# Kernel optimization log

Measured on AMD Instinct MI355X. Metric: run time of the kernel, lower is better.

The kernel has to match this reference:

```python
import jax, jax.numpy as jnp
import numpy as np


def _maxpool2x2(t):
    # t: [B, C, H, W] -> [B, C, H//2, W//2]
    b, c, h, w = t.shape
    return t.reshape(b, c, h // 2, 2, w // 2, 2).max(axis=(3, 5))


def setup_inputs() -> dict:
    key = jax.random.key(0)
    ks = jax.random.split(key, 6)
    B, C, H, W = 16, 64, 64, 64
    x = jax.random.normal(ks[0], (B, C, H, W), dtype=jnp.float32)
    # 1x1 conv weights (no bias), stored as [out_ch, in_ch]
    s = 0.05
    W_theta = jax.random.normal(ks[1], (C // 8, C), dtype=jnp.float32) * s
    W_phi = jax.random.normal(ks[2], (C // 8, C), dtype=jnp.float32) * s
    W_g = jax.random.normal(ks[3], (C // 2, C), dtype=jnp.float32) * s
    W_attn = jax.random.normal(ks[4], (C, C // 2), dtype=jnp.float32) * s
    sigma = jnp.ones((1,), dtype=jnp.float32) * 0.5  # nonzero so attn path matters
    return {"x": x, "W_theta": W_theta, "W_phi": W_phi, "W_g": W_g,
            "W_attn": W_attn, "sigma": sigma}


def reference(x, W_theta, W_phi, W_g, W_attn, sigma):
    B, C, H, W = x.shape
    N = H * W
    M = N // 4
    # 1x1 convs are channel matmuls
    theta = jnp.einsum('oc,bchw->bohw', W_theta, x).reshape(B, C // 8, N)      # [B, C/8, N]
    phi = _maxpool2x2(jnp.einsum('oc,bchw->bohw', W_phi, x)).reshape(B, C // 8, M)  # [B, C/8, M]
    attn = jax.nn.softmax(jnp.einsum('bkn,bkm->bnm', theta, phi), axis=-1)    # [B, N, M]
    g = _maxpool2x2(jnp.einsum('oc,bchw->bohw', W_g, x)).reshape(B, C // 2, M)  # [B, C/2, M]
    attn_g = jnp.einsum('bgm,bnm->bgn', g, attn).reshape(B, C // 2, H, W)      # [B, C/2, H, W]
    attn_g = jnp.einsum('oc,bchw->bohw', W_attn, attn_g)                        # [B, C, H, W]
    return x + sigma * attn_g
```

## Files before the change

kernel.cpp:

```cpp
#include <hip/hip_runtime.h>
#include <hip/hip_bf16.h>

#define CC 64
#define NN 4096
#define MM 1024

typedef __attribute__((ext_vector_type(4))) short s4b;
typedef __attribute__((ext_vector_type(8))) short s8b;
typedef __attribute__((ext_vector_type(4))) float float4v;

__device__ inline unsigned short f2bf(float f) {
    union { float f; unsigned u; } v; v.f = f;
    unsigned r = v.u + 0x7fff + ((v.u >> 16) & 1);
    return (unsigned short)(r >> 16);
}

__device__ inline float4v mfma16(s4b a, s4b b, float4v c) {
#if __has_builtin(__builtin_amdgcn_mfma_f32_16x16x16bf16_1k)
    return __builtin_amdgcn_mfma_f32_16x16x16bf16_1k(a, b, c, 0, 0, 0);
#else
    float4v d;
    asm volatile("v_mfma_f32_16x16x16_bf16 %0, %1, %2, %3"
                 : "=v"(d) : "v"(a), "v"(b), "v"(c));
    return d;
#endif
}

__device__ inline float4v mfma32(s8b a, s8b b, float4v c) {
#if __has_builtin(__builtin_amdgcn_mfma_f32_16x16x32_bf16)
    return __builtin_amdgcn_mfma_f32_16x16x32_bf16(a, b, c, 0, 0, 0);
#else
    float4v d;
    asm volatile("v_mfma_f32_16x16x32_bf16 %0, %1, %2, %3"
                 : "=v"(d) : "v"(a), "v"(b), "v"(c));
    return d;
#endif
}

__global__ __launch_bounds__(256) void prep_kernel(
    const float* __restrict__ x,
    const float* __restrict__ Wth,
    const float* __restrict__ Wph,
    const float* __restrict__ Wg,
    unsigned short* __restrict__ thT,
    unsigned short* __restrict__ phiP,
    unsigned short* __restrict__ gP)
{
    __shared__ float wt[64 * 48];
    __shared__ float buf[128 * 49];

    const int tid  = threadIdx.x;
    const int b    = blockIdx.y;
    const int hp   = blockIdx.x;
    const int pix  = tid & 127;
    const int half = tid >> 7;

    for (int idx = tid; idx < 64 * 48; idx += 256) {
        const int c = idx / 48, j = idx % 48;
        float v;
        if (j < 8)       v = Wth[j * 64 + c];
        else if (j < 16) v = Wph[(j - 8) * 64 + c];
        else             v = Wg[(j - 16) * 64 + c];
        wt[c * 48 + j] = v;
    }
    __syncthreads();

    const int n = (2 * hp + (pix >> 6)) * 64 + (pix & 63);
    const float* xb = x + (size_t)b * CC * NN + (size_t)half * 32 * NN + n;

    float acc[48];
#pragma unroll
    for (int j = 0; j < 48; ++j) acc[j] = 0.f;

#pragma unroll
    for (int c0 = 0; c0 < 32; c0 += 16) {
        float xv[16];
#pragma unroll
        for (int u = 0; u < 16; ++u) xv[u] = xb[(size_t)(c0 + u) * NN];
#pragma unroll
        for (int u = 0; u < 16; ++u) {
            const float* wrow = &wt[(half * 32 + c0 + u) * 48];
#pragma unroll
            for (int j = 0; j < 48; ++j) acc[j] += wrow[j] * xv[u];
        }
    }

    if (half == 1) {
#pragma unroll
        for (int j = 0; j < 48; ++j) buf[pix * 49 + j] = acc[j];
    }
    __syncthreads();

    if (half == 0) {
#pragma unroll
        for (int j = 0; j < 48; ++j) acc[j] += buf[pix * 49 + j];
        union { unsigned short s[8]; uint4 v; } pk;
#pragma unroll
        for (int j = 0; j < 8; ++j) pk.s[j] = f2bf(acc[j] * 1.44269504f);
        *(uint4*)&thT[((size_t)b * NN + n) * 8] = pk.v;
#pragma unroll
        for (int j = 0; j < 40; ++j) buf[pix * 49 + j] = acc[8 + j];
    }
    __syncthreads();

    for (int idx = tid; idx < 1280; idx += 256) {
        const int pm = idx & 31;
        const int j  = idx >> 5;
        const int p00 = 2 * pm, p10 = 64 + 2 * pm;
        const float v = fmaxf(fmaxf(buf[p00 * 49 + j], buf[(p00 + 1) * 49 + j]),
                              fmaxf(buf[p10 * 49 + j], buf[(p10 + 1) * 49 + j]));
        const int m = hp * 32 + pm;
        if (j < 8) phiP[((size_t)b * MM + m) * 8 + j] = f2bf(v);
        else       gP[((size_t)b * 32 + (j - 8)) * MM + m] = f2bf(v);
    }
}

__global__ __launch_bounds__(256) void attn_mfma(
    const unsigned short* __restrict__ thT,
    const unsigned short* __restrict__ phiP,
    const unsigned short* __restrict__ gP,
    const float* __restrict__ x,
    const float* __restrict__ Wa,
    const float* __restrict__ sigma,
    float* __restrict__ out)
{
    constexpr int GP = 264;
    constexpr int OBP = 40;

    __shared__ __align__(16) union {
        struct {
            unsigned short phi[256 * 8 + 16];
            unsigned short g[32 * GP];
        } m;
        struct {
            float part[18][128];
            unsigned short obb[64 * OBP];
        } cb;
    } sh;

    const int tid  = threadIdx.x;
    const int lane = tid & 63;
    const int wv   = tid >> 6;
    const int wq   = wv & 1;
    const int wk   = wv >> 1;
    const int c15  = lane & 15;
    const int quad = lane >> 4;
    const int b    = blockIdx.y;
    const int n0   = blockIdx.x * 64;

    union { unsigned short s[8]; s8b v; } wfrag;
    {
        const float* wr = Wa + (wv * 16 + c15) * 32 + quad * 8;
        const float4 w0 = *(const float4*)wr;
        const float4 w1 = *(const float4*)(wr + 4);
        wfrag.s[0] = f2bf(w0.x); wfrag.s[1] = f2bf(w0.y);
        wfrag.s[2] = f2bf(w0.z); wfrag.s[3] = f2bf(w0.w);
        wfrag.s[4] = f2bf(w1.x); wfrag.s[5] = f2bf(w1.y);
        wfrag.s[6] = f2bf(w1.z); wfrag.s[7] = f2bf(w1.w);
    }

    s4b zero4 = {0, 0, 0, 0};
    s4b bthA = zero4, bthB = zero4;
    if (quad < 2) {
        union { uint2 u; s4b s; } t;
        t.u = *(const uint2*)&thT[((size_t)b * NN + n0 + wq * 32 + c15) * 8 + quad * 4];
        bthA = t.s;
        t.u = *(const uint2*)&thT[((size_t)b * NN + n0 + wq * 32 + 16 + c15) * 8 + quad * 4];
        bthB = t.s;
    }

    float4v accA0 = {0.f, 0.f, 0.f, 0.f};
    float4v accA1 = {0.f, 0.f, 0.f, 0.f};
    float4v accB0 = {0.f, 0.f, 0.f, 0.f};
    float4v accB1 = {0.f, 0.f, 0.f, 0.f};
    float zaccA = 0.f, zaccB = 0.f;

    const int wk4 = wk * 4;

    for (int ch = 0; ch < 4; ++ch) {
        __syncthreads();
        {
            const int r  = tid & 7;
            const int q3 = (tid >> 3) & 3;
            const int slot = (tid & ~31) | ((r >> 2) << 4) | (q3 << 2) | (r & 3);
            *(uint4*)&sh.m.phi[slot * 8] =
                *(const uint4*)&phiP[((size_t)b * MM + ch * 256 + tid) * 8];
            if (tid < 2) {
                uint4 z4; z4.x = z4.y = z4.z = z4.w = 0u;
                *(uint4*)&sh.m.phi[256 * 8 + tid * 8] = z4;
            }
        }
#pragma unroll
        for (int it = 0; it < 4; ++it) {
            const int idx = tid + 256 * it;
            const int grow = idx >> 5, c32 = idx & 31;
            *(uint4*)&sh.m.g[grow * GP + c32 * 8] =
                *(const uint4*)&gP[((size_t)b * 32 + grow) * MM + ch * 256 + c32 * 8];
        }
        __syncthreads();

        const unsigned short* pA  = &sh.m.phi[c15 * 8 + quad * 4];
        const unsigned short* pg0 = &sh.m.g[c15 * GP + quad * 8];
        const unsigned short* pg1 = pg0 + 16 * GP;

#pragma unroll
        for (int s = 0; s < 4; ++s) {
            const int g32 = wk4 + s;

            union { uint2 u; s4b s_; } apA, apB;
            apA.u = *(const uint2*)&pA[g32 * 256];
            apB.u = *(const uint2*)&pA[g32 * 256 + 128];

            float4v cz = {0.f, 0.f, 0.f, 0.f};
            float4v sAlo = mfma16(apA.s_, bthA, cz);
            float4v sAhi = mfma16(apB.s_, bthA, cz);
            float4v sBlo = mfma16(apA.s_, bthB, cz);
            float4v sBhi = mfma16(apB.s_, bthB, cz);

            union { float f; unsigned u; } a0, a1, a2, a3, b0, b1, b2, b3;
            a0.f = __builtin_amdgcn_exp2f(sAlo[0]);
            a1.f = __builtin_amdgcn_exp2f(sAlo[1]);
            a2.f = __builtin_amdgcn_exp2f(sAlo[2]);
            a3.f = __builtin_amdgcn_exp2f(sAlo[3]);
            b0.f = __builtin_amdgcn_exp2f(sAhi[0]);
            b1.f = __builtin_amdgcn_exp2f(sAhi[1]);
            b2.f = __builtin_amdgcn_exp2f(sAhi[2]);
            b3.f = __builtin_amdgcn_exp2f(sAhi[3]);
            zaccA += ((a0.f + a1.f) + (a2.f + a3.f)) +
                     ((b0.f + b1.f) + (b2.f + b3.f));
            union { uint4 u; s8b s_; } paA;
            paA.u.x = __builtin_amdgcn_perm(a1.u, a0.u, 0x07060302u);
            paA.u.y = __builtin_amdgcn_perm(a3.u, a2.u, 0x07060302u);
            paA.u.z = __builtin_amdgcn_perm(b1.u, b0.u, 0x07060302u);
            paA.u.w = __builtin_amdgcn_perm(b3.u, b2.u, 0x07060302u);

            a0.f = __builtin_amdgcn_exp2f(sBlo[0]);
            a1.f = __builtin_amdgcn_exp2f(sBlo[1]);
            a2.f = __builtin_amdgcn_exp2f(sBlo[2]);
            a3.f = __builtin_amdgcn_exp2f(sBlo[3]);
            b0.f = __builtin_amdgcn_exp2f(sBhi[0]);
            b1.f = __builtin_amdgcn_exp2f(sBhi[1]);
            b2.f = __builtin_amdgcn_exp2f(sBhi[2]);
            b3.f = __builtin_amdgcn_exp2f(sBhi[3]);
            zaccB += ((a0.f + a1.f) + (a2.f + a3.f)) +
                     ((b0.f + b1.f) + (b2.f + b3.f));
            union { uint4 u; s8b s_; } paB;
            paB.u.x = __builtin_amdgcn_perm(a1.u, a0.u, 0x07060302u);
            paB.u.y = __builtin_amdgcn_perm(a3.u, a2.u, 0x07060302u);
            paB.u.z = __builtin_amdgcn_perm(b1.u, b0.u, 0x07060302u);
            paB.u.w = __builtin_amdgcn_perm(b3.u, b2.u, 0x07060302u);

            union { uint4 u; s8b s_; } bg0, bg1;
            bg0.u = *(const uint4*)&pg0[g32 * 32];
            bg1.u = *(const uint4*)&pg1[g32 * 32];

            accA0 = mfma32(paA.s_, bg0.s_, accA0);
            accA1 = mfma32(paA.s_, bg1.s_, accA1);
            accB0 = mfma32(paB.s_, bg0.s_, accB0);
            accB1 = mfma32(paB.s_, bg1.s_, accB1);
        }
    }

    __syncthreads();
    if (wk == 1) {
#pragma unroll
        for (int r = 0; r < 4; ++r) {
            sh.cb.part[     r][wq * 64 + lane] = accA0[r];
            sh.cb.part[ 4 + r][wq * 64 + lane] = accA1[r];
            sh.cb.part[ 8 + r][wq * 64 + lane] = accB0[r];
            sh.cb.part[12 + r][wq * 64 + lane] = accB1[r];
        }
        sh.cb.part[16][wq * 64 + lane] = zaccA;
        sh.cb.part[17][wq * 64 + lane] = zaccB;
    }
    __syncthreads();

    if (wk == 0) {
#pragma unroll
        for (int r = 0; r < 4; ++r) {
            accA0[r] += sh.cb.part[     r][wq * 64 + lane];
            accA1[r] += sh.cb.part[ 4 + r][wq * 64 + lane];
            accB0[r] += sh.cb.part[ 8 + r][wq * 64 + lane];
            accB1[r] += sh.cb.part[12 + r][wq * 64 + lane];
        }
        zaccA += sh.cb.part[16][wq * 64 + lane];
        zaccB += sh.cb.part[17][wq * 64 + lane];

        float zA = zaccA, zB = zaccB;
        zA += __shfl_xor(zA, 16, 64);
        zA += __shfl_xor(zA, 32, 64);
        zB += __shfl_xor(zB, 16, 64);
        zB += __shfl_xor(zB, 32, 64);
        const float rzqA = __builtin_amdgcn_rcpf(zA);
        const float rzqB = __builtin_amdgcn_rcpf(zB);

#pragma unroll
        for (int r = 0; r < 4; ++r) {
            const float rzA = __shfl(rzqA, quad * 4 + r, 64);
            const float rzB = __shfl(rzqB, quad * 4 + r, 64);
            const int qlA = wq * 32 + quad * 4 + r;
            const int qlB = qlA + 16;
            sh.cb.obb[qlA * OBP + c15]      = f2bf(accA0[r] * rzA);
            sh.cb.obb[qlA * OBP + 16 + c15] = f2bf(accA1[r] * rzA);
            sh.cb.obb[qlB * OBP + c15]      = f2bf(accB0[r] * rzB);
            sh.cb.obb[qlB * OBP + 16 + c15] = f2bf(accB1[r] * rzB);
        }
    }
    __syncthreads();

    const float sg = sigma[0];
#pragma unroll
    for (int t = 0; t < 4; ++t) {
        union { uint4 u; s8b s_; } bo;
        bo.u = *(const uint4*)&sh.cb.obb[(t * 16 + c15) * OBP + quad * 8];
        float4v cz = {0.f, 0.f, 0.f, 0.f};
        float4v oc = mfma32(wfrag.v, bo.s_, cz);
#pragma unroll
        for (int r = 0; r < 4; ++r) {
            const size_t oi = ((size_t)b * CC + wv * 16 + quad * 4 + r) * NN
                              + n0 + t * 16 + c15;
            out[oi] = x[oi] + sg * oc[r];
        }
    }
}

extern "C" void kernel_launch(void* const* d_in, const int* in_sizes, int n_in,
                              void* d_out, int out_size, void* d_ws, size_t ws_size,
                              hipStream_t stream) {
    const float* x      = (const float*)d_in[0];
    const float* W_th   = (const float*)d_in[1];
    const float* W_ph   = (const float*)d_in[2];
    const float* W_g    = (const float*)d_in[3];
    const float* W_attn = (const float*)d_in[4];
    const float* sigma  = (const float*)d_in[5];
    float* out = (float*)d_out;

    const int B = 16;
    unsigned short* thT  = (unsigned short*)d_ws;
    unsigned short* phiP = thT + (size_t)B * NN * 8;
    unsigned short* gP   = phiP + (size_t)B * MM * 8;

    prep_kernel<<<dim3(32, 16), 256, 0, stream>>>(x, W_th, W_ph, W_g,
                                                  thT, phiP, gP);
    attn_mfma<<<dim3(64, 16), 256, 0, stream>>>(thT, phiP, gP, x,
                                                W_attn, sigma, out);
}
```

Baseline: 106.0 us.

## Compute prep-kernel 1x1 projections with bf16 MFMA instead of scalar FMA

```diff
diff --git a/kernel.cpp b/kernel.cpp
--- a/kernel.cpp
+++ b/kernel.cpp
@@ -46,72 +46,115 @@
     unsigned short* __restrict__ phiP,
     unsigned short* __restrict__ gP)
 {
-    __shared__ float wt[64 * 48];
-    __shared__ float buf[128 * 49];
+    constexpr int XP = 72;
+    constexpr int DP = 49;
+
+    __shared__ __align__(16) union {
+        unsigned short xs[128 * XP];
+        float bufD[128 * DP];
+    } sh;
 
     const int tid  = threadIdx.x;
     const int b    = blockIdx.y;
     const int hp   = blockIdx.x;
-    const int pix  = tid & 127;
-    const int half = tid >> 7;
-
-    for (int idx = tid; idx < 64 * 48; idx += 256) {
-        const int c = idx / 48, j = idx % 48;
-        float v;
-        if (j < 8)       v = Wth[j * 64 + c];
-        else if (j < 16) v = Wph[(j - 8) * 64 + c];
-        else             v = Wg[(j - 16) * 64 + c];
-        wt[c * 48 + j] = v;
-    }
-    __syncthreads();
-
-    const int n = (2 * hp + (pix >> 6)) * 64 + (pix & 63);
-    const float* xb = x + (size_t)b * CC * NN + (size_t)half * 32 * NN + n;
-
-    float acc[48];
-#pragma unroll
-    for (int j = 0; j < 48; ++j) acc[j] = 0.f;
-
-#pragma unroll
-    for (int c0 = 0; c0 < 32; c0 += 16) {
-        float xv[16];
-#pragma unroll
-        for (int u = 0; u < 16; ++u) xv[u] = xb[(size_t)(c0 + u) * NN];
-#pragma unroll
-        for (int u = 0; u < 16; ++u) {
-            const float* wrow = &wt[(half * 32 + c0 + u) * 48];
-#pragma unroll
-            for (int j = 0; j < 48; ++j) acc[j] += wrow[j] * xv[u];
-        }
-    }
-
-    if (half == 1) {
-#pragma unroll
-        for (int j = 0; j < 48; ++j) buf[pix * 49 + j] = acc[j];
-    }
-    __syncthreads();
-
-    if (half == 0) {
-#pragma unroll
-        for (int j = 0; j < 48; ++j) acc[j] += buf[pix * 49 + j];
-        union { unsigned short s[8]; uint4 v; } pk;
-#pragma unroll
-        for (int j = 0; j < 8; ++j) pk.s[j] = f2bf(acc[j] * 1.44269504f);
-        *(uint4*)&thT[((size_t)b * NN + n) * 8] = pk.v;
-#pragma unroll
-        for (int j = 0; j < 40; ++j) buf[pix * 49 + j] = acc[8 + j];
-    }
-    __syncthreads();
+    const int lane = tid & 63;
+    const int wv   = tid >> 6;
+    const int c15  = lane & 15;
+    const int quad = lane >> 4;
+    const int n0row = hp * 128;
+
+    s8b wf[3][2];
+    {
+        const float* base0 = (c15 < 8) ? (Wth + c15 * 64)
+                                       : (Wph + (c15 - 8) * 64);
+        const float* base1 = Wg + c15 * 64;
+        const float* base2 = Wg + (16 + c15) * 64;
+        const float* bases[3] = {base0, base1, base2};
+#pragma unroll
+        for (int t = 0; t < 3; ++t) {
+#pragma unroll
+            for (int s = 0; s < 2; ++s) {
+                const float* p = bases[t] + s * 32 + quad * 8;
+                const float4 w0 = *(const float4*)p;
+                const float4 w1 = *(const float4*)(p + 4);
+                union { unsigned short us[8]; s8b v; } tmp;
+                tmp.us[0] = f2bf(w0.x); tmp.us[1] = f2bf(w0.y);
+                tmp.us[2] = f2bf(w0.z); tmp.us[3] = f2bf(w0.w);
+                tmp.us[4] = f2bf(w1.x); tmp.us[5] = f2bf(w1.y);
+                tmp.us[6] = f2bf(w1.z); tmp.us[7] = f2bf(w1.w);
+                wf[t][s] = tmp.v;
+            }
+        }
+    }
+
+    {
+        const int spx = tid & 127;
+        const int chp = tid >> 7;
+        const float* xb = x + (size_t)b * CC * NN + n0row + spx;
+#pragma unroll
+        for (int i = 0; i < 16; ++i) {
+            const int c0 = i * 4 + chp * 2;
+            const float va = xb[(size_t)c0 * NN];
+            const float vb = xb[(size_t)(c0 + 1) * NN];
+            const unsigned pk = (unsigned)f2bf(va) |
+                                ((unsigned)f2bf(vb) << 16);
+            *(unsigned*)&sh.xs[spx * XP + c0] = pk;
+        }
+    }
+    __syncthreads();
+
+    float4v acc[2][3];
+#pragma unroll
+    for (int tl = 0; tl < 2; ++tl)
+#pragma unroll
+        for (int t = 0; t < 3; ++t)
+            acc[tl][t] = float4v{0.f, 0.f, 0.f, 0.f};
+
+#pragma unroll
+    for (int tl = 0; tl < 2; ++tl) {
+        const int p0 = wv * 32 + tl * 16;
+#pragma unroll
+        for (int s = 0; s < 2; ++s) {
+            union { uint4 u; s8b v; } bx;
+            bx.u = *(const uint4*)&sh.xs[(p0 + c15) * XP + s * 32 + quad * 8];
+#pragma unroll
+            for (int t = 0; t < 3; ++t)
+                acc[tl][t] = mfma32(wf[t][s], bx.v, acc[tl][t]);
+        }
+    }
+    __syncthreads();
+
+#pragma unroll
+    for (int tl = 0; tl < 2; ++tl) {
+        const int p0 = wv * 32 + tl * 16;
+#pragma unroll
+        for (int t = 0; t < 3; ++t)
+#pragma unroll
+            for (int r = 0; r < 4; ++r)
+                sh.bufD[(p0 + c15) * DP + t * 16 + quad * 4 + r]
+                    = acc[tl][t][r];
+    }
+    __syncthreads();
+
+    if (tid < 128) {
+        const int px = tid;
+        union { unsigned short s_[8]; uint4 v; } pk;
+#pragma unroll
+        for (int j = 0; j < 8; ++j)
+            pk.s_[j] = f2bf(sh.bufD[px * DP + j] * 1.44269504f);
+        *(uint4*)&thT[((size_t)b * NN + n0row + px) * 8] = pk.v;
+    }
 
     for (int idx = tid; idx < 1280; idx += 256) {
         const int pm = idx & 31;
-        const int j  = idx >> 5;
+        const int jj = idx >> 5;
         const int p00 = 2 * pm, p10 = 64 + 2 * pm;
-        const float v = fmaxf(fmaxf(buf[p00 * 49 + j], buf[(p00 + 1) * 49 + j]),
-                              fmaxf(buf[p10 * 49 + j], buf[(p10 + 1) * 49 + j]));
+        const float v = fmaxf(
+            fmaxf(sh.bufD[p00 * DP + 8 + jj], sh.bufD[(p00 + 1) * DP + 8 + jj]),
+            fmaxf(sh.bufD[p10 * DP + 8 + jj], sh.bufD[(p10 + 1) * DP + 8 + jj]));
         const int m = hp * 32 + pm;
-        if (j < 8) phiP[((size_t)b * MM + m) * 8 + j] = f2bf(v);
-        else       gP[((size_t)b * 32 + (j - 8)) * MM + m] = f2bf(v);
+        if (jj < 8) phiP[((size_t)b * MM + m) * 8 + jj] = f2bf(v);
+        else        gP[((size_t)b * 32 + (jj - 8)) * MM + m] = f2bf(v);
     }
 }
 
```

Result: faster. 99.72 us (-6.0%).
